# Performance work log

Measured on AMD Instinct MI355X. Metric: run time of the kernel, lower is better.

## Reference

```python
import jax, jax.numpy as jnp
import numpy as np

GAMMA = 0.999      # EMA momentum
M_PROTO = 10       # prototypes per class
K_CLS = 201        # 200 classes + background
EPS_SK = 0.05      # sinkhorn temperature
SK_ITERS = 3       # sinkhorn iterations
THR = 0.5          # pseudo-gt threshold
D_BB = 768         # backbone dim
D = 512            # projected dim


def _ln(x, g, b, eps=1e-5):
    mu = x.mean(-1, keepdims=True)
    var = ((x - mu) ** 2).mean(-1, keepdims=True)
    return (x - mu) / jnp.sqrt(var + eps) * g + b


def _l2n(x, eps=1e-12):
    n = jnp.linalg.norm(x, axis=-1, keepdims=True)
    return x / jnp.maximum(n, eps)


def _pca_dir(A, niter=10):
    # rank-1 PCA direction (deterministic power iteration; mirrors torch.pca_lowrank(q=1, center=True))
    Ac = A - A.mean(0, keepdims=True)
    v = jnp.ones((A.shape[1],), A.dtype) / jnp.sqrt(jnp.asarray(A.shape[1], A.dtype))
    for _ in range(niter):
        v = Ac.T @ (Ac @ v)
        v = v / jnp.linalg.norm(v)
    u = Ac @ v
    return u / jnp.linalg.norm(u)


def setup_inputs() -> dict:
    key = jax.random.key(0)
    ks = jax.random.split(key, 6)
    B, HW = 16, 1024
    return dict(
        patch_tokens=jax.random.normal(ks[0], (B, HW, D_BB), jnp.float32),
        gt=jax.random.randint(ks[1], (B,), 0, K_CLS - 1),
        proj_w=jax.random.normal(ks[2], (D, D_BB), jnp.float32) * 0.02,
        proj_b=jnp.zeros((D,), jnp.float32),
        feat_g=jnp.ones((D,), jnp.float32),
        feat_b=jnp.zeros((D,), jnp.float32),
        mask_g=jnp.ones((K_CLS,), jnp.float32),
        mask_b=jnp.zeros((K_CLS,), jnp.float32),
        prototypes=jax.random.normal(ks[3], (K_CLS, M_PROTO, D), jnp.float32) * 0.02,
    )


def reference(patch_tokens, gt, proj_w, proj_b, feat_g, feat_b, mask_g, mask_b, prototypes):
    B, HW, _ = patch_tokens.shape
    H = W = int(np.sqrt(HW))
    N = B * HW

    # ----- ged_pseudo_gt (on detached tokens) -----
    U = _pca_dir(patch_tokens.reshape(-1, D_BB))            # [N]
    Us = (U - U.min()) / (U.max() - U.min())
    Us = Us.reshape(B, H, W)
    pseudo_gt = jnp.where(Us < THR, gt[:, None, None], K_CLS - 1)  # [B,H,W]

    # ----- projection + normalization -----
    f = patch_tokens @ proj_w.T + proj_b                    # [B,HW,D]
    _c = _l2n(_ln(f.reshape(N, D), feat_g, feat_b))         # [N,D]
    protos = _l2n(prototypes)                               # buffer is l2-normalized in-place
    masks = jnp.einsum('nd,kmd->nmk', _c, protos)           # [N,M,K] cosine sims
    out_flat = _ln(masks.max(axis=1), mask_g, mask_b)       # [N,K]
    out_seg = out_flat.reshape(B, H, W, K_CLS).transpose(0, 3, 1, 2)  # [B,K,H,W]

    # ----- prototype_learning (vectorized 201-class loop) -----
    gt_seg = pseudo_gt.reshape(-1)                          # [N] int
    pred = jnp.argmax(out_flat, axis=-1)
    correct = (gt_seg == pred).astype(_c.dtype)             # [N]
    proto_logits = _c @ protos.reshape(-1, D).T             # [N, K*M]

    sel = jax.nn.one_hot(gt_seg, K_CLS, dtype=_c.dtype)     # [N,K] class membership
    Bk = sel.sum(0)                                         # pixels per class
    Bk_safe = jnp.where(Bk > 0, Bk, 1.0)

    # masked per-class sinkhorn (all classes in parallel)
    Q = jnp.exp(masks / EPS_SK) * sel[:, None, :]           # [N,M,K]
    sQ = Q.sum((0, 1))                                      # [K]
    Q = Q / jnp.where(sQ > 0, sQ, 1.0)
    for _ in range(SK_ITERS):
        row = Q.sum(0, keepdims=True)                       # [1,M,K] sum over pixels
        Q = Q / jnp.where(row > 0, row, 1.0) / M_PROTO
        col = Q.sum(1, keepdims=True)                       # [N,1,K] sum over prototypes
        Q = Q / jnp.where(col > 0, col, 1.0) / Bk_safe
    Q = Q * Bk                                              # [N,M,K]

    Qn = jnp.take_along_axis(Q, gt_seg[:, None, None], axis=2)[:, :, 0]  # [N,M]
    idx = jnp.argmax(Qn, axis=1)                            # hard assignment per pixel
    proto_target = (idx + M_PROTO * gt_seg).astype(jnp.float32)

    # EMA update: q masked by prediction correctness (m_k applies to both m_q and c_q; m_k^2 = m_k)
    q = jax.nn.one_hot(idx, M_PROTO, dtype=_c.dtype) * correct[:, None]  # [N,M]
    fproto = jnp.einsum('nk,nm,nd->kmd', sel, q, _c)        # per-(class,proto) feature sums
    ncnt = jnp.einsum('nk,nm->km', sel, q)                  # assignment counts
    fnorm = _l2n(fproto)
    upd = (ncnt != 0)[:, :, None]
    new_protos = _l2n(jnp.where(upd, GAMMA * protos + (1.0 - GAMMA) * fnorm, protos))

    return out_seg, proto_logits, proto_target, pseudo_gt, new_protos
```

## Files before the change

kernel.cpp:

```cpp
#include <hip/hip_runtime.h>
#include <cstdint>
#include <cstddef>

typedef _Float16 half8  __attribute__((ext_vector_type(8)));
typedef _Float16 half4v __attribute__((ext_vector_type(4)));
typedef float    f32x4  __attribute__((ext_vector_type(4)));

static constexpr int HWPX = 1024;
static constexpr int NPX  = 16384;
static constexpr int DBB  = 768;
static constexpr int DD   = 512;
static constexpr int KC   = 201;
static constexpr int KM   = 2010;
static constexpr int KMP  = 2048;

static constexpr size_t OFF_MEANP  = 0;
static constexpr size_t OFF_XCH    = 49152;
static constexpr size_t OFF_ROW16  = 540672;
static constexpr size_t OFF_ROW3   = 669696;
static constexpr size_t OFF_ROW5   = 677760;
static constexpr size_t OFF_BK     = 685824;
static constexpr size_t OFF_NCNT   = 686848;
static constexpr size_t OFF_FPROTO = 694912;
static constexpr size_t ZTOTAL     = 4811392;
static constexpr size_t OFF_MSF    = 4811392;
static constexpr size_t OFF_GTSEG  = 4817536;
static constexpr size_t OFF_CORR   = 4883072;
static constexpr size_t OFF_U      = 4948608;
static constexpr size_t OFF_PN     = 5079680;
static constexpr size_t OFF_P16    = 9196160;
static constexpr size_t OFF_C16    = 11293312;
static constexpr size_t OFF_QD     = 28070528;
static constexpr size_t OFF_W16    = 28725888;

static constexpr size_t OUT_SEG = 0;
static constexpr size_t OUT_PL  = 3293184;
static constexpr size_t OUT_PT  = 36225024;
static constexpr size_t OUT_PG  = 36241408;
static constexpr size_t OUT_NP  = 36257792;

#define GLDS16(gp, lp) __builtin_amdgcn_global_load_lds( \
    (__attribute__((address_space(1))) const void*)(gp), \
    (__attribute__((address_space(3))) void*)(lp), 16, 0, 0)

static __device__ __forceinline__ float  wredf(float x){
  #pragma unroll
  for (int o=32;o;o>>=1) x += __shfl_down(x,o);
  return x;
}
static __device__ __forceinline__ double wredd(double x){
  #pragma unroll
  for (int o=32;o;o>>=1) x += __shfl_down(x,o);
  return x;
}

__global__ __launch_bounds__(256) void kP0(const float* __restrict__ A, double* __restrict__ meanp){
  __shared__ double red[4][12][64];
  int lane = threadIdx.x & 63, w = threadIdx.x >> 6;
  int rbase = blockIdx.x*16 + w*4;
  double acc[12];
  #pragma unroll
  for (int j=0;j<12;j++) acc[j]=0.0;
  for (int i=0;i<4;i++){
    const float* Ar = A + (size_t)(rbase+i)*DBB;
    #pragma unroll
    for (int j=0;j<12;j++) acc[j] += (double)Ar[j*64+lane];
  }
  #pragma unroll
  for (int j=0;j<12;j++) red[w][j][lane] = acc[j];
  __syncthreads();
  double* dst = meanp + (size_t)(blockIdx.x&7)*768;
  for (int cc=threadIdx.x; cc<768; cc+=256){
    int j = cc>>6, l = cc&63;
    atomicAdd(&dst[cc], red[0][j][l]+red[1][j][l]+red[2][j][l]+red[3][j][l]);
  }
}

__global__ __launch_bounds__(256) void kRedM(const double* __restrict__ meanp, double* __restrict__ msf){
  for (int cc=threadIdx.x; cc<768; cc+=256){
    double s=0.0;
    #pragma unroll
    for (int p=0;p<8;p++) s += meanp[p*768+cc];
    msf[cc] = s * (1.0/16384.0);
  }
}

__global__ __launch_bounds__(256) void kPIter(const float* __restrict__ A, const double* __restrict__ msf,
                                              const double* __restrict__ xp, double* __restrict__ y){
  __shared__ double vs[768], ms[768];
  __shared__ double red[4][12][64];
  for (int cc=threadIdx.x; cc<768; cc+=256){
    ms[cc] = msf[cc];
    if (xp){
      double sv=0.0;
      #pragma unroll
      for (int p=0;p<8;p++) sv += xp[p*768+cc];
      vs[cc] = sv;
    } else {
      vs[cc] = 1.0/sqrt(768.0);
    }
  }
  __syncthreads();
  int lane = threadIdx.x & 63, w = threadIdx.x >> 6;
  int rbase = blockIdx.x*16 + w*4;
  double acc[12];
  #pragma unroll
  for (int j=0;j<12;j++) acc[j]=0.0;
  for (int i=0;i<4;i++){
    const float* Ar = A + (size_t)(rbase+i)*DBB;
    double ad[12]; double wp = 0.0;
    #pragma unroll
    for (int j=0;j<12;j++){ int c=j*64+lane; ad[j] = (double)Ar[c]-ms[c]; wp += ad[j]*vs[c]; }
    wp = wredd(wp); wp = __shfl(wp, 0);
    #pragma unroll
    for (int j=0;j<12;j++) acc[j] += wp*ad[j];
  }
  #pragma unroll
  for (int j=0;j<12;j++) red[w][j][lane] = acc[j];
  __syncthreads();
  double* dst = y + (size_t)(blockIdx.x&7)*768;
  for (int cc=threadIdx.x; cc<768; cc+=256){
    int j = cc>>6, l = cc&63;
    atomicAdd(&dst[cc], red[0][j][l]+red[1][j][l]+red[2][j][l]+red[3][j][l]);
  }
}

__global__ __launch_bounds__(256) void kPU(const float* __restrict__ A, const double* __restrict__ msf,
                                           const double* __restrict__ vp, double* __restrict__ u){
  __shared__ double vs[768], ms[768];
  for (int cc=threadIdx.x; cc<768; cc+=256){
    ms[cc] = msf[cc];
    double sv=0.0;
    #pragma unroll
    for (int p=0;p<8;p++) sv += vp[p*768+cc];
    vs[cc] = sv;
  }
  __syncthreads();
  int lane=threadIdx.x&63, w=threadIdx.x>>6;
  int rbase = blockIdx.x*16 + w*4;
  for (int i=0;i<4;i++){
    const float* Ar = A + (size_t)(rbase+i)*DBB;
    double wp=0.0;
    #pragma unroll
    for (int j=0;j<12;j++){ int c=j*64+lane; wp += ((double)Ar[c]-ms[c])*vs[c]; }
    wp = wredd(wp);
    if (lane==0) u[rbase+i] = wp;
  }
}

__global__ __launch_bounds__(1024) void kFin(const double* __restrict__ u, const int* __restrict__ gt,
      float* __restrict__ outPG, int* __restrict__ gtseg, int* __restrict__ Bk){
  __shared__ double smn[16], smx[16];
  __shared__ double sres[2];
  int t = threadIdx.x;
  double mn=1e300, mx=-1e300;
  for (int k=0;k<16;k++){ double x=u[k*1024+t]; mn=fmin(mn,x); mx=fmax(mx,x); }
  #pragma unroll
  for (int o=32;o;o>>=1){ mn=fmin(mn,__shfl_down(mn,o)); mx=fmax(mx,__shfl_down(mx,o)); }
  if ((t&63)==0){ smn[t>>6]=mn; smx[t>>6]=mx; }
  __syncthreads();
  if (t==0){
    for (int i=1;i<16;i++){ mn=fmin(mn,smn[i]); mx=fmax(mx,smx[i]); }
    sres[0]=mn; sres[1]=mx;
  }
  __syncthreads();
  mn=sres[0]; mx=sres[1];
  double inv = 1.0/(mx-mn);
  for (int k=0;k<16;k++){
    int n = k*1024 + t;
    int c0 = gt[k];
    double us = (u[n]-mn)*inv;
    int g = (us < 0.5) ? c0 : 200;
    outPG[n] = (float)g;
    gtseg[n] = g;
    unsigned long long b0 = __ballot(g==c0);
    unsigned long long b1 = __ballot(g==200);
    if ((t&63)==0){
      atomicAdd(&Bk[c0], (int)__popcll(b0));
      atomicAdd(&Bk[200], (int)__popcll(b1));
    }
  }
}

__global__ __launch_bounds__(256) void kPrep(const float* __restrict__ Wp, _Float16* __restrict__ W16,
    const float* __restrict__ PR, float* __restrict__ Pn, _Float16* __restrict__ P16){
  int b = blockIdx.x;
  if (b < 384){
    int i = b*256 + threadIdx.x;
    float4 vv = ((const float4*)Wp)[i];
    half4v h; h[0]=(_Float16)vv.x; h[1]=(_Float16)vv.y; h[2]=(_Float16)vv.z; h[3]=(_Float16)vv.w;
    ((half4v*)W16)[i] = h;
    return;
  }
  int w=threadIdx.x>>6, lane=threadIdx.x&63;
  int km = (b-384)*4 + w;
  if (km >= KM){
    if (km < KMP){
      half8 z;
      #pragma unroll
      for (int i=0;i<8;i++) z[i]=(_Float16)0.0f;
      *(half8*)(P16 + (size_t)km*DD + lane*8) = z;
    }
    return;
  }
  const float* r = PR + (size_t)km*DD + lane*8;
  float4 a = *(const float4*)r, b2 = *(const float4*)(r+4);
  float x[8] = {a.x,a.y,a.z,a.w,b2.x,b2.y,b2.z,b2.w};
  float ss=0;
  #pragma unroll
  for (int i=0;i<8;i++) ss += x[i]*x[i];
  ss = __shfl(wredf(ss),0);
  float nrm = fmaxf(sqrtf(ss), 1e-12f);
  float* pw = Pn + (size_t)km*DD + lane*8;
  half8 h;
  #pragma unroll
  for (int i=0;i<8;i++){ float vv = x[i]/nrm; pw[i]=vv; h[i]=(_Float16)vv; }
  *(half8*)(P16 + (size_t)km*DD + lane*8) = h;
}

__global__ __launch_bounds__(256) void gemm1(const float* __restrict__ Af, const _Float16* __restrict__ Bm,
    _Float16* __restrict__ Ch, const float* __restrict__ bias){
  __shared__ __align__(16) char As[128*128];
  __shared__ __align__(16) char Bs[128*128];
  const int tid = threadIdx.x;
  const int lane = tid & 63, w = tid >> 6;
  const int wr = w >> 1, wc = w & 1;
  const int lrow = lane & 15, kg = lane >> 4;
  const int id = blockIdx.x;
  const int xcd = id & 7, pos = id >> 3;
  const int m0 = ((xcd<<4) | (pos>>2)) * 128;
  const int n0 = (pos & 3) * 128;

  f32x4 acc[4][4];
  #pragma unroll
  for (int i=0;i<4;i++)
    #pragma unroll
    for (int j=0;j<4;j++){ f32x4 z = {0.f,0.f,0.f,0.f}; acc[i][j]=z; }

  for (int k0 = 0; k0 < DBB; k0 += 64){
    #pragma unroll
    for (int i=0;i<4;i++){
      int slot = (i*4 + w)*64 + lane;
      int r = slot >> 3, c = slot & 7;
      int cs = c ^ (r & 7);
      GLDS16(Bm + (size_t)(n0+r)*DBB + k0 + cs*8, Bs + (i*4+w)*1024);
    }
    #pragma unroll
    for (int i=0;i<8;i++){
      int slot = i*256 + tid;
      int r = slot >> 4, c4 = slot & 15;
      float4 v = *(const float4*)(Af + (size_t)(m0+r)*DBB + k0 + c4*4);
      half4v h; h[0]=(_Float16)v.x; h[1]=(_Float16)v.y; h[2]=(_Float16)v.z; h[3]=(_Float16)v.w;
      *(half4v*)(As + r*128 + (((c4>>1)^(r&7))<<4) + (c4&1)*8) = h;
    }
    __syncthreads();
    #pragma unroll
    for (int h=0; h<2; h++){
      half8 af[4], bf[4];
      #pragma unroll
      for (int mi=0;mi<4;mi++){
        int ar = wr*64 + mi*16 + lrow;
        af[mi] = *(const half8*)(As + ar*128 + (((h*4+kg) ^ (ar&7))<<4));
      }
      #pragma unroll
      for (int nj=0;nj<4;nj++){
        int br = wc*64 + nj*16 + lrow;
        bf[nj] = *(const half8*)(Bs + br*128 + (((h*4+kg) ^ (br&7))<<4));
      }
      #pragma unroll
      for (int mi=0;mi<4;mi++)
        #pragma unroll
        for (int nj=0;nj<4;nj++)
          acc[mi][nj] = __builtin_amdgcn_mfma_f32_16x16x32_f16(af[mi], bf[nj], acc[mi][nj], 0,0,0);
    }
    __syncthreads();
  }
  #pragma unroll
  for (int mi=0;mi<4;mi++){
    int gr = m0 + wr*64 + mi*16 + kg*4;
    #pragma unroll
    for (int nj=0;nj<4;nj++){
      int gc = n0 + wc*64 + nj*16 + lrow;
      float bv = bias[gc];
      #pragma unroll
      for (int r2=0;r2<4;r2++)
        Ch[(size_t)(gr+r2)*DD + gc] = (_Float16)(acc[mi][nj][r2] + bv);
    }
  }
}

__global__ __launch_bounds__(256) void gemm2(const _Float16* __restrict__ Am, const _Float16* __restrict__ Bm,
    float* __restrict__ Cf){
  __shared__ __align__(16) char As[128*128];
  __shared__ __align__(16) char Bs[128*128];
  const int tid = threadIdx.x;
  const int lane = tid & 63, w = tid >> 6;
  const int wr = w >> 1, wc = w & 1;
  const int lrow = lane & 15, kg = lane >> 4;
  const int id = blockIdx.x;
  const int xcd = id & 7, pos = id >> 3;
  const int m0 = ((xcd<<4) | (pos>>4)) * 128;
  const int n0 = (pos & 15) * 128;

  f32x4 acc[4][4];
  #pragma unroll
  for (int i=0;i<4;i++)
    #pragma unroll
    for (int j=0;j<4;j++){ f32x4 z = {0.f,0.f,0.f,0.f}; acc[i][j]=z; }

  for (int k0 = 0; k0 < DD; k0 += 64){
    #pragma unroll
    for (int i=0;i<4;i++){
      int slot = (i*4 + w)*64 + lane;
      int r = slot >> 3, c = slot & 7;
      int cs = c ^ (r & 7);
      GLDS16(Am + (size_t)(m0+r)*DD + k0 + cs*8, As + (i*4+w)*1024);
      GLDS16(Bm + (size_t)(n0+r)*DD + k0 + cs*8, Bs + (i*4+w)*1024);
    }
    __syncthreads();
    #pragma unroll
    for (int h=0; h<2; h++){
      half8 af[4], bf[4];
      #pragma unroll
      for (int mi=0;mi<4;mi++){
        int ar = wr*64 + mi*16 + lrow;
        af[mi] = *(const half8*)(As + ar*128 + (((h*4+kg) ^ (ar&7))<<4));
      }
      #pragma unroll
      for (int nj=0;nj<4;nj++){
        int br = wc*64 + nj*16 + lrow;
        bf[nj] = *(const half8*)(Bs + br*128 + (((h*4+kg) ^ (br&7))<<4));
      }
      #pragma unroll
      for (int mi=0;mi<4;mi++)
        #pragma unroll
        for (int nj=0;nj<4;nj++)
          acc[mi][nj] = __builtin_amdgcn_mfma_f32_16x16x32_f16(af[mi], bf[nj], acc[mi][nj], 0,0,0);
    }
    __syncthreads();
  }
  #pragma unroll
  for (int mi=0;mi<4;mi++){
    int gr = m0 + wr*64 + mi*16 + kg*4;
    #pragma unroll
    for (int nj=0;nj<4;nj++){
      int gc = n0 + wc*64 + nj*16 + lrow;
      if (gc < KM){
        #pragma unroll
        for (int r2=0;r2<4;r2++)
          Cf[(size_t)(gr+r2)*KM + gc] = acc[mi][nj][r2];
      }
    }
  }
}

__global__ __launch_bounds__(256) void kLNl2n(_Float16* __restrict__ C16,
      const float* __restrict__ fg, const float* __restrict__ fb){
  int w=threadIdx.x>>6, lane=threadIdx.x&63;
  int n = blockIdx.x*4 + w;
  _Float16* row = C16 + (size_t)n*DD + lane*8;
  half8 h = *(const half8*)row;
  float x[8];
  #pragma unroll
  for (int i=0;i<8;i++) x[i] = (float)h[i];
  float s=0;
  #pragma unroll
  for (int i=0;i<8;i++) s += x[i];
  float mu = __shfl(wredf(s),0)/512.f;
  float q=0;
  #pragma unroll
  for (int i=0;i<8;i++){ float d=x[i]-mu; q+=d*d; }
  float var = __shfl(wredf(q),0)/512.f;
  float inv = 1.f/sqrtf(var+1e-5f);
  float4 g0 = *(const float4*)(fg+lane*8), g1 = *(const float4*)(fg+lane*8+4);
  float4 b0 = *(const float4*)(fb+lane*8), b1 = *(const float4*)(fb+lane*8+4);
  float gg[8] = {g0.x,g0.y,g0.z,g0.w,g1.x,g1.y,g1.z,g1.w};
  float bb[8] = {b0.x,b0.y,b0.z,b0.w,b1.x,b1.y,b1.z,b1.w};
  float y[8]; float ss=0;
  #pragma unroll
  for (int i=0;i<8;i++){ y[i] = (x[i]-mu)*inv*gg[i]+bb[i]; ss += y[i]*y[i]; }
  float nrm = fmaxf(sqrtf(__shfl(wredf(ss),0)), 1e-12f);
  half8 o;
  #pragma unroll
  for (int i=0;i<8;i++) o[i] = (_Float16)(y[i]/nrm);
  *(half8*)row = o;
}

__global__ __launch_bounds__(256) void kMaxSK(const float* __restrict__ PL, const float* __restrict__ mg,
    const float* __restrict__ mb, const int* __restrict__ gtseg, const int* __restrict__ gt,
    float* __restrict__ outseg, int* __restrict__ corr, float* __restrict__ Qd, float* __restrict__ row16){
  __shared__ float rowb[4][2016];
  __shared__ float tile[32][205];
  int w=threadIdx.x>>6, lane=threadIdx.x&63;
  int n0 = blockIdx.x*32;
  int b = n0>>10, hw0 = n0&1023;
  int c0 = gt[b];
  float p0=0.f, p1=0.f;
  for (int g8=0; g8<8; ++g8){
    int n = n0 + g8*4 + w;
    int g = gtseg[n];
    const float* src = PL + (size_t)n*KM;
    for (int j2=lane;j2<1005;j2+=64)
      *(float2*)(&rowb[w][j2*2]) = *(const float2*)(src + j2*2);
    float xv[4]; int ncl=0;
    for (int c=lane;c<KC;c+=64){
      float mx = rowb[w][c*10];
      #pragma unroll
      for (int m=1;m<10;m++) mx = fmaxf(mx, rowb[w][c*10+m]);
      xv[ncl++] = mx;
    }
    float ps=0;
    for (int i=0;i<ncl;i++) ps += xv[i];
    float mu = __shfl(wredf(ps),0)*(1.f/201.f);
    float pv=0;
    for (int i=0;i<ncl;i++){ float d=xv[i]-mu; pv+=d*d; }
    float var = __shfl(wredf(pv),0)*(1.f/201.f);
    float inv = 1.f/sqrtf(var+1e-5f);
    float bv = -3.0e38f; int bi = 1<<30;
    int lr = g8*4 + w;
    ncl = 0;
    for (int c=lane;c<KC;c+=64){
      float o = (xv[ncl]-mu)*inv*mg[c]+mb[c]; ncl++;
      tile[lr][c] = o;
      if (o > bv){ bv=o; bi=c; }
    }
    #pragma unroll
    for (int o2=32;o2;o2>>=1){
      float ov = __shfl_down(bv,o2); int oi = __shfl_down(bi,o2);
      if (ov>bv || (ov==bv && oi<bi)){ bv=ov; bi=oi; }
    }
    if (lane==0) corr[n] = (bi==gtseg[n]) ? 1 : 0;
    if (lane < 10){
      float e = expf(rowb[w][g*10+lane]*20.f);
      Qd[(size_t)n*10+lane] = e;
      if (g==c0) p0 += e; else p1 += e;
    }
  }
  if (lane < 10){
    float* rp = row16 + (size_t)(blockIdx.x&15)*2016 + lane*KC;
    atomicAdd(&rp[c0], p0);
    atomicAdd(&rp[200], p1);
  }
  __syncthreads();
  for (int idx=threadIdx.x; idx<KC*32; idx+=256){
    int c = idx>>5, j = idx&31;
    outseg[(((size_t)b*KC+c)<<10) + hw0 + j] = tile[j][c];
  }
}

__global__ __launch_bounds__(256) void kSKpass(float* __restrict__ Qd, const int* __restrict__ gtseg,
      const int* __restrict__ gt, const float* __restrict__ rin, int rin_parts,
      float* __restrict__ rout, const int* __restrict__ Bk){
  __shared__ float rin2[10][2];
  __shared__ double part[4][10][2];
  int n = blockIdx.x*256+threadIdx.x;
  int c0 = gt[blockIdx.x>>2];
  if (threadIdx.x < 20){
    int m = threadIdx.x>>1, cl = threadIdx.x&1;
    int cls = cl?200:c0;
    float s=0;
    for (int p=0;p<rin_parts;p++) s += rin[(size_t)p*2016 + m*KC + cls];
    rin2[m][cl]=s;
  }
  __syncthreads();
  int g = gtseg[n];
  int cl = (g==200)?1:0;
  double q[10]; double col=0.0;
  #pragma unroll
  for (int m=0;m<10;m++){
    double r = (double)rin2[m][cl];
    double t = (double)Qd[(size_t)n*10+m];
    if (r>0.0) t = t/r;
    t = t/10.0;
    q[m]=t; col+=t;
  }
  double cs = (col>0.0)? col : 1.0;
  int bk = Bk[g];
  double bs = (bk>0)? (double)bk : 1.0;
  double inv = 1.0/(cs*bs);
  int w=threadIdx.x>>6, lane=threadIdx.x&63;
  #pragma unroll
  for (int m=0;m<10;m++){
    double t = q[m]*inv;
    Qd[(size_t)n*10+m] = (float)t;
    double p0 = (g==c0)? t:0.0;
    double p1 = (g==200)? t:0.0;
    p0=wredd(p0); p1=wredd(p1);
    if (lane==0){ part[w][m][0]=p0; part[w][m][1]=p1; }
  }
  __syncthreads();
  if (threadIdx.x < 20){
    int m = threadIdx.x>>1, cl2 = threadIdx.x&1;
    double t = part[0][m][cl2]+part[1][m][cl2]+part[2][m][cl2]+part[3][m][cl2];
    atomicAdd(&rout[m*KC + (cl2?200:c0)], (float)t);
  }
}

__global__ __launch_bounds__(256) void kSKEMA(const float* __restrict__ Qd, const int* __restrict__ gtseg,
      const float* __restrict__ r5, const int* __restrict__ corr, const _Float16* __restrict__ C16,
      float* __restrict__ outPT, float* __restrict__ fproto, int* __restrict__ ncnt){
  int w=threadIdx.x>>6, lane=threadIdx.x&63;
  int n = blockIdx.x*4+w;
  int g = gtseg[n];
  float tv = -1.0f;
  if (lane<10){
    float r = r5[lane*KC+g];
    float t = Qd[(size_t)n*10+lane];
    if (r>0.f) t = t/r;
    tv = t*0.1f;
  }
  float bv = tv; int bi = lane;
  #pragma unroll
  for (int o=8;o;o>>=1){
    float ov = __shfl_down(bv,o); int oi = __shfl_down(bi,o);
    if (ov>bv || (ov==bv && oi<bi)){ bv=ov; bi=oi; }
  }
  bi = __shfl(bi, 0);
  if (lane==0) outPT[n] = (float)(bi + 10*g);
  if (corr[n]){
    half8 hc = *(const half8*)(C16 + (size_t)n*DD + lane*8);
    float* dst = fproto + ((size_t)g*10+bi)*DD + lane*8;
    #pragma unroll
    for (int i=0;i<8;i++) atomicAdd(dst+i, (float)hc[i]);
    if (lane==0) atomicAdd(&ncnt[g*10+bi], 1);
  }
}

__global__ __launch_bounds__(256) void kEMAfin(const float* __restrict__ fproto, const int* __restrict__ ncnt,
     const float* __restrict__ Pn, float* __restrict__ outNP){
  int w=threadIdx.x>>6, lane=threadIdx.x&63;
  int km = blockIdx.x*4+w;
  if (km>=KM) return;
  const float* fr = fproto + (size_t)km*DD + lane*8;
  float fp[8]; float ss=0;
  #pragma unroll
  for (int i=0;i<8;i++){ fp[i]=fr[i]; ss+=fp[i]*fp[i]; }
  float n1 = fmaxf(sqrtf(__shfl(wredf(ss),0)), 1e-12f);
  int cnt = ncnt[km];
  const float* pr = Pn + (size_t)km*DD + lane*8;
  float t[8]; float s2=0;
  #pragma unroll
  for (int i=0;i<8;i++){
    float pv = pr[i];
    float tv = cnt ? (0.999f*pv + 0.001f*(fp[i]/n1)) : pv;
    t[i]=tv; s2+=tv*tv;
  }
  float n2 = fmaxf(sqrtf(__shfl(wredf(s2),0)), 1e-12f);
  float* dst = outNP + (size_t)km*DD + lane*8;
  #pragma unroll
  for (int i=0;i<8;i++) dst[i] = t[i]/n2;
}

extern "C" void kernel_launch(void* const* d_in, const int* in_sizes, int n_in,
                              void* d_out, int out_size, void* d_ws, size_t ws_size,
                              hipStream_t stream) {
  const float* A   = (const float*)d_in[0];
  const int*   gt  = (const int*)d_in[1];
  const float* Wp  = (const float*)d_in[2];
  const float* pb  = (const float*)d_in[3];
  const float* fg  = (const float*)d_in[4];
  const float* fb  = (const float*)d_in[5];
  const float* mg  = (const float*)d_in[6];
  const float* mb  = (const float*)d_in[7];
  const float* PR  = (const float*)d_in[8];
  float* out = (float*)d_out;
  char* ws = (char*)d_ws;

  double* meanp  = (double*)(ws+OFF_MEANP);
  double* xch    = (double*)(ws+OFF_XCH);
  float*  row16  = (float*)(ws+OFF_ROW16);
  float*  row3   = (float*)(ws+OFF_ROW3);
  float*  row5   = (float*)(ws+OFF_ROW5);
  int*    Bk     = (int*)(ws+OFF_BK);
  int*    ncnt   = (int*)(ws+OFF_NCNT);
  float*  fproto = (float*)(ws+OFF_FPROTO);
  double* msf    = (double*)(ws+OFF_MSF);
  int*    gtseg  = (int*)(ws+OFF_GTSEG);
  int*    corr   = (int*)(ws+OFF_CORR);
  double* u      = (double*)(ws+OFF_U);
  float*  Pn     = (float*)(ws+OFF_PN);
  _Float16* P16  = (_Float16*)(ws+OFF_P16);
  _Float16* C16  = (_Float16*)(ws+OFF_C16);
  float*  Qd     = (float*)(ws+OFF_QD);
  _Float16* W16  = (_Float16*)(ws+OFF_W16);

  hipMemsetAsync(ws, 0, ZTOTAL, stream);

  kP0<<<1024,256,0,stream>>>(A, meanp);
  kRedM<<<1,256,0,stream>>>(meanp, msf);
  for (int t=0;t<10;t++){
    const double* xp = (t==0)? nullptr : (xch + (size_t)(t-1)*8*768);
    kPIter<<<1024,256,0,stream>>>(A, msf, xp, xch + (size_t)t*8*768);
  }
  kPU<<<1024,256,0,stream>>>(A, msf, xch + (size_t)9*8*768, u);
  kFin<<<1,1024,0,stream>>>(u, gt, out+OUT_PG, gtseg, Bk);

  kPrep<<<896,256,0,stream>>>(Wp, W16, PR, Pn, P16);

  gemm1<<<512,256,0,stream>>>(A, W16, C16, pb);
  kLNl2n<<<4096,256,0,stream>>>(C16, fg, fb);

  gemm2<<<2048,256,0,stream>>>(C16, P16, out+OUT_PL);

  kMaxSK<<<512,256,0,stream>>>(out+OUT_PL, mg, mb, gtseg, gt, out+OUT_SEG, corr, Qd, row16);

  kSKpass<<<64,256,0,stream>>>(Qd, gtseg, gt, row16, 16, row3, Bk);
  kSKpass<<<64,256,0,stream>>>(Qd, gtseg, gt, row3, 1, row5, Bk);
  kSKEMA<<<4096,256,0,stream>>>(Qd, gtseg, row5, corr, C16, out+OUT_PT, fproto, ncnt);

  kEMAfin<<<503,256,0,stream>>>(fproto, ncnt, Pn, out+OUT_NP);
}
```

Measured before the change: 394.9 us.

## Fold mean-centering into power iteration and restructure max-pool kernel

```diff
diff --git a/kernel.cpp b/kernel.cpp
--- a/kernel.cpp
+++ b/kernel.cpp
@@ -14,24 +14,24 @@
 static constexpr int KM   = 2010;
 static constexpr int KMP  = 2048;
 
-static constexpr size_t OFF_MEANP  = 0;
-static constexpr size_t OFF_XCH    = 49152;
-static constexpr size_t OFF_ROW16  = 540672;
-static constexpr size_t OFF_ROW3   = 669696;
-static constexpr size_t OFF_ROW5   = 677760;
-static constexpr size_t OFF_BK     = 685824;
-static constexpr size_t OFF_NCNT   = 686848;
-static constexpr size_t OFF_FPROTO = 694912;
-static constexpr size_t ZTOTAL     = 4811392;
-static constexpr size_t OFF_MSF    = 4811392;
-static constexpr size_t OFF_GTSEG  = 4817536;
-static constexpr size_t OFF_CORR   = 4883072;
-static constexpr size_t OFF_U      = 4948608;
-static constexpr size_t OFF_PN     = 5079680;
-static constexpr size_t OFF_P16    = 9196160;
-static constexpr size_t OFF_C16    = 11293312;
-static constexpr size_t OFF_QD     = 28070528;
-static constexpr size_t OFF_W16    = 28725888;
+static constexpr size_t OFF_XCH    = 0;
+static constexpr size_t OFF_TP     = 491520;
+static constexpr size_t OFF_COLP   = 492160;
+static constexpr size_t OFF_ROW16  = 541312;
+static constexpr size_t OFF_ROW3   = 670336;
+static constexpr size_t OFF_ROW5   = 678400;
+static constexpr size_t OFF_BK     = 686464;
+static constexpr size_t OFF_NCNT   = 687488;
+static constexpr size_t OFF_FPROTO = 695552;
+static constexpr size_t ZTOTAL     = 4812032;
+static constexpr size_t OFF_GTSEG  = 4812032;
+static constexpr size_t OFF_CORR   = 4877568;
+static constexpr size_t OFF_U      = 4943104;
+static constexpr size_t OFF_PN     = 5074176;
+static constexpr size_t OFF_P16    = 9190656;
+static constexpr size_t OFF_C16    = 11287808;
+static constexpr size_t OFF_QD     = 28065024;
+static constexpr size_t OFF_W16    = 28720384;
 
 static constexpr size_t OUT_SEG = 0;
 static constexpr size_t OUT_PL  = 3293184;
@@ -54,97 +54,99 @@
   return x;
 }
 
-__global__ __launch_bounds__(256) void kP0(const float* __restrict__ A, double* __restrict__ meanp){
+template<bool FIRST>
+__global__ __launch_bounds__(256) void kPIter2(const float* __restrict__ A,
+    const double* __restrict__ Win, const double* __restrict__ Tin, const double* __restrict__ colp,
+    double* __restrict__ Wout, double* __restrict__ Tout, double* __restrict__ colout){
+  __shared__ double vs[768];
   __shared__ double red[4][12][64];
-  int lane = threadIdx.x & 63, w = threadIdx.x >> 6;
+  __shared__ double sT[4];
+  int tid=threadIdx.x, lane=tid&63, w=tid>>6;
+  if (FIRST){
+    for (int cc=tid; cc<768; cc+=256) vs[cc] = 1.0/sqrt(768.0);
+  } else {
+    double Ts=0.0;
+    #pragma unroll
+    for (int p=0;p<8;p++) Ts += Tin[p];
+    for (int cc=tid; cc<768; cc+=256){
+      double sw=0.0, mc=0.0;
+      #pragma unroll
+      for (int p=0;p<8;p++){ sw += Win[p*768+cc]; mc += colp[p*768+cc]; }
+      vs[cc] = sw - mc*(1.0/16384.0)*Ts;
+    }
+  }
+  __syncthreads();
   int rbase = blockIdx.x*16 + w*4;
-  double acc[12];
-  #pragma unroll
-  for (int j=0;j<12;j++) acc[j]=0.0;
+  double acc[12], cacc[12]; double tloc=0.0;
+  #pragma unroll
+  for (int j=0;j<12;j++){ acc[j]=0.0; cacc[j]=0.0; }
   for (int i=0;i<4;i++){
     const float* Ar = A + (size_t)(rbase+i)*DBB;
-    #pragma unroll
-    for (int j=0;j<12;j++) acc[j] += (double)Ar[j*64+lane];
-  }
-  #pragma unroll
-  for (int j=0;j<12;j++) red[w][j][lane] = acc[j];
-  __syncthreads();
-  double* dst = meanp + (size_t)(blockIdx.x&7)*768;
-  for (int cc=threadIdx.x; cc<768; cc+=256){
-    int j = cc>>6, l = cc&63;
+    double a[12]; double wp=0.0;
+    #pragma unroll
+    for (int j=0;j<12;j++){ int c=j*64+lane; a[j]=(double)Ar[c]; wp += a[j]*vs[c]; }
+    wp = wredd(wp); wp = __shfl(wp,0);
+    #pragma unroll
+    for (int j=0;j<12;j++) acc[j] += wp*a[j];
+    if (FIRST){
+      #pragma unroll
+      for (int j=0;j<12;j++) cacc[j] += a[j];
+    }
+    tloc += wp;
+  }
+  #pragma unroll
+  for (int j=0;j<12;j++) red[w][j][lane]=acc[j];
+  if (lane==0) sT[w]=tloc;
+  __syncthreads();
+  double* dst = Wout + (size_t)(blockIdx.x&7)*768;
+  for (int cc=tid; cc<768; cc+=256){
+    int j=cc>>6, l=cc&63;
     atomicAdd(&dst[cc], red[0][j][l]+red[1][j][l]+red[2][j][l]+red[3][j][l]);
   }
-}
-
-__global__ __launch_bounds__(256) void kRedM(const double* __restrict__ meanp, double* __restrict__ msf){
-  for (int cc=threadIdx.x; cc<768; cc+=256){
-    double s=0.0;
-    #pragma unroll
-    for (int p=0;p<8;p++) s += meanp[p*768+cc];
-    msf[cc] = s * (1.0/16384.0);
-  }
-}
-
-__global__ __launch_bounds__(256) void kPIter(const float* __restrict__ A, const double* __restrict__ msf,
-                                              const double* __restrict__ xp, double* __restrict__ y){
-  __shared__ double vs[768], ms[768];
-  __shared__ double red[4][12][64];
-  for (int cc=threadIdx.x; cc<768; cc+=256){
-    ms[cc] = msf[cc];
-    if (xp){
-      double sv=0.0;
-      #pragma unroll
-      for (int p=0;p<8;p++) sv += xp[p*768+cc];
-      vs[cc] = sv;
-    } else {
-      vs[cc] = 1.0/sqrt(768.0);
-    }
-  }
-  __syncthreads();
-  int lane = threadIdx.x & 63, w = threadIdx.x >> 6;
-  int rbase = blockIdx.x*16 + w*4;
-  double acc[12];
-  #pragma unroll
-  for (int j=0;j<12;j++) acc[j]=0.0;
-  for (int i=0;i<4;i++){
-    const float* Ar = A + (size_t)(rbase+i)*DBB;
-    double ad[12]; double wp = 0.0;
-    #pragma unroll
-    for (int j=0;j<12;j++){ int c=j*64+lane; ad[j] = (double)Ar[c]-ms[c]; wp += ad[j]*vs[c]; }
-    wp = wredd(wp); wp = __shfl(wp, 0);
-    #pragma unroll
-    for (int j=0;j<12;j++) acc[j] += wp*ad[j];
-  }
-  #pragma unroll
-  for (int j=0;j<12;j++) red[w][j][lane] = acc[j];
-  __syncthreads();
-  double* dst = y + (size_t)(blockIdx.x&7)*768;
-  for (int cc=threadIdx.x; cc<768; cc+=256){
-    int j = cc>>6, l = cc&63;
-    atomicAdd(&dst[cc], red[0][j][l]+red[1][j][l]+red[2][j][l]+red[3][j][l]);
-  }
-}
-
-__global__ __launch_bounds__(256) void kPU(const float* __restrict__ A, const double* __restrict__ msf,
-                                           const double* __restrict__ vp, double* __restrict__ u){
-  __shared__ double vs[768], ms[768];
-  for (int cc=threadIdx.x; cc<768; cc+=256){
-    ms[cc] = msf[cc];
-    double sv=0.0;
-    #pragma unroll
-    for (int p=0;p<8;p++) sv += vp[p*768+cc];
-    vs[cc] = sv;
-  }
-  __syncthreads();
-  int lane=threadIdx.x&63, w=threadIdx.x>>6;
+  if (tid==0) atomicAdd(&Tout[blockIdx.x&7], sT[0]+sT[1]+sT[2]+sT[3]);
+  if (FIRST){
+    __syncthreads();
+    #pragma unroll
+    for (int j=0;j<12;j++) red[w][j][lane]=cacc[j];
+    __syncthreads();
+    double* cdst = colout + (size_t)(blockIdx.x&7)*768;
+    for (int cc=tid; cc<768; cc+=256){
+      int j=cc>>6, l=cc&63;
+      atomicAdd(&cdst[cc], red[0][j][l]+red[1][j][l]+red[2][j][l]+red[3][j][l]);
+    }
+  }
+}
+
+__global__ __launch_bounds__(256) void kPU2(const float* __restrict__ A, const double* __restrict__ Wp,
+    const double* __restrict__ Tp, const double* __restrict__ colp, double* __restrict__ u){
+  __shared__ double vs[768];
+  __shared__ double sS[4];
+  int tid=threadIdx.x, lane=tid&63, w=tid>>6;
+  double Ts=0.0;
+  #pragma unroll
+  for (int p=0;p<8;p++) Ts += Tp[p];
+  double sloc=0.0;
+  for (int cc=tid; cc<768; cc+=256){
+    double sw=0.0, mc=0.0;
+    #pragma unroll
+    for (int p=0;p<8;p++){ sw += Wp[p*768+cc]; mc += colp[p*768+cc]; }
+    double m = mc*(1.0/16384.0);
+    double v = sw - m*Ts;
+    vs[cc] = v;
+    sloc += m*v;
+  }
+  sloc = wredd(sloc);
+  if (lane==0) sS[w]=sloc;
+  __syncthreads();
+  double s = sS[0]+sS[1]+sS[2]+sS[3];
   int rbase = blockIdx.x*16 + w*4;
   for (int i=0;i<4;i++){
     const float* Ar = A + (size_t)(rbase+i)*DBB;
     double wp=0.0;
     #pragma unroll
-    for (int j=0;j<12;j++){ int c=j*64+lane; wp += ((double)Ar[c]-ms[c])*vs[c]; }
+    for (int j=0;j<12;j++){ int c=j*64+lane; wp += (double)Ar[c]*vs[c]; }
     wp = wredd(wp);
-    if (lane==0) u[rbase+i] = wp;
+    if (lane==0) u[rbase+i] = wp - s;
   }
 }
 
@@ -389,26 +391,46 @@
 __global__ __launch_bounds__(256) void kMaxSK(const float* __restrict__ PL, const float* __restrict__ mg,
     const float* __restrict__ mb, const int* __restrict__ gtseg, const int* __restrict__ gt,
     float* __restrict__ outseg, int* __restrict__ corr, float* __restrict__ Qd, float* __restrict__ row16){
-  __shared__ float rowb[4][2016];
-  __shared__ float tile[32][205];
-  int w=threadIdx.x>>6, lane=threadIdx.x&63;
-  int n0 = blockIdx.x*32;
+  __shared__ float tile[16][205];
+  __shared__ float qpart[10][2];
+  int tid=threadIdx.x, lane=tid&63, w=tid>>6;
+  int n0 = blockIdx.x*16;
   int b = n0>>10, hw0 = n0&1023;
   int c0 = gt[b];
-  float p0=0.f, p1=0.f;
-  for (int g8=0; g8<8; ++g8){
-    int n = n0 + g8*4 + w;
+  if (tid<20) qpart[tid>>1][tid&1]=0.f;
+  __syncthreads();
+  for (int r=0;r<16;r++){
+    int n = n0 + r;
     int g = gtseg[n];
-    const float* src = PL + (size_t)n*KM;
-    for (int j2=lane;j2<1005;j2+=64)
-      *(float2*)(&rowb[w][j2*2]) = *(const float2*)(src + j2*2);
+    if (tid < KC){
+      const float* src = PL + (size_t)n*KM + tid*10;
+      float v[10];
+      #pragma unroll
+      for (int m2=0;m2<5;m2++){
+        float2 t2 = *(const float2*)(src + m2*2);
+        v[m2*2]=t2.x; v[m2*2+1]=t2.y;
+      }
+      float mx = v[0];
+      #pragma unroll
+      for (int m=1;m<10;m++) mx = fmaxf(mx,v[m]);
+      tile[r][tid] = mx;
+      if (tid == g){
+        int cl = (g==200)?1:0;
+        #pragma unroll
+        for (int m=0;m<10;m++){
+          float e = expf(v[m]*20.f);
+          Qd[(size_t)n*10+m] = e;
+          atomicAdd(&qpart[m][cl], e);
+        }
+      }
+    }
+  }
+  __syncthreads();
+  for (int rr=0; rr<4; ++rr){
+    int r = w*4 + rr;
+    int n = n0 + r;
     float xv[4]; int ncl=0;
-    for (int c=lane;c<KC;c+=64){
-      float mx = rowb[w][c*10];
-      #pragma unroll
-      for (int m=1;m<10;m++) mx = fmaxf(mx, rowb[w][c*10+m]);
-      xv[ncl++] = mx;
-    }
+    for (int c=lane;c<KC;c+=64) xv[ncl++] = tile[r][c];
     float ps=0;
     for (int i=0;i<ncl;i++) ps += xv[i];
     float mu = __shfl(wredf(ps),0)*(1.f/201.f);
@@ -416,34 +438,27 @@
     for (int i=0;i<ncl;i++){ float d=xv[i]-mu; pv+=d*d; }
     float var = __shfl(wredf(pv),0)*(1.f/201.f);
     float inv = 1.f/sqrtf(var+1e-5f);
-    float bv = -3.0e38f; int bi = 1<<30;
-    int lr = g8*4 + w;
-    ncl = 0;
+    float bv=-3.0e38f; int bi=1<<30;
+    ncl=0;
     for (int c=lane;c<KC;c+=64){
       float o = (xv[ncl]-mu)*inv*mg[c]+mb[c]; ncl++;
-      tile[lr][c] = o;
-      if (o > bv){ bv=o; bi=c; }
+      tile[r][c] = o;
+      if (o>bv){ bv=o; bi=c; }
     }
     #pragma unroll
     for (int o2=32;o2;o2>>=1){
-      float ov = __shfl_down(bv,o2); int oi = __shfl_down(bi,o2);
-      if (ov>bv || (ov==bv && oi<bi)){ bv=ov; bi=oi; }
-    }
-    if (lane==0) corr[n] = (bi==gtseg[n]) ? 1 : 0;
-    if (lane < 10){
-      float e = expf(rowb[w][g*10+lane]*20.f);
-      Qd[(size_t)n*10+lane] = e;
-      if (g==c0) p0 += e; else p1 += e;
-    }
-  }
-  if (lane < 10){
-    float* rp = row16 + (size_t)(blockIdx.x&15)*2016 + lane*KC;
-    atomicAdd(&rp[c0], p0);
-    atomicAdd(&rp[200], p1);
-  }
-  __syncthreads();
-  for (int idx=threadIdx.x; idx<KC*32; idx+=256){
-    int c = idx>>5, j = idx&31;
+      float ov=__shfl_down(bv,o2); int oi=__shfl_down(bi,o2);
+      if (ov>bv||(ov==bv&&oi<bi)){bv=ov;bi=oi;}
+    }
+    if (lane==0) corr[n] = (bi==gtseg[n])?1:0;
+  }
+  __syncthreads();
+  if (tid<20){
+    int m=tid>>1, cl=tid&1;
+    atomicAdd(&row16[(size_t)(blockIdx.x&15)*2016 + m*KC + (cl?200:c0)], qpart[m][cl]);
+  }
+  for (int idx=tid; idx<KC*16; idx+=256){
+    int c=idx>>4, j=idx&15;
     outseg[(((size_t)b*KC+c)<<10) + hw0 + j] = tile[j][c];
   }
 }
@@ -566,15 +581,15 @@
   float* out = (float*)d_out;
   char* ws = (char*)d_ws;
 
-  double* meanp  = (double*)(ws+OFF_MEANP);
   double* xch    = (double*)(ws+OFF_XCH);
+  double* Tp     = (double*)(ws+OFF_TP);
+  double* colp   = (double*)(ws+OFF_COLP);
   float*  row16  = (float*)(ws+OFF_ROW16);
   float*  row3   = (float*)(ws+OFF_ROW3);
   float*  row5   = (float*)(ws+OFF_ROW5);
   int*    Bk     = (int*)(ws+OFF_BK);
   int*    ncnt   = (int*)(ws+OFF_NCNT);
   float*  fproto = (float*)(ws+OFF_FPROTO);
-  double* msf    = (double*)(ws+OFF_MSF);
   int*    gtseg  = (int*)(ws+OFF_GTSEG);
   int*    corr   = (int*)(ws+OFF_CORR);
   double* u      = (double*)(ws+OFF_U);
@@ -586,13 +601,13 @@
 
   hipMemsetAsync(ws, 0, ZTOTAL, stream);
 
-  kP0<<<1024,256,0,stream>>>(A, meanp);
-  kRedM<<<1,256,0,stream>>>(meanp, msf);
-  for (int t=0;t<10;t++){
-    const double* xp = (t==0)? nullptr : (xch + (size_t)(t-1)*8*768);
-    kPIter<<<1024,256,0,stream>>>(A, msf, xp, xch + (size_t)t*8*768);
-  }
-  kPU<<<1024,256,0,stream>>>(A, msf, xch + (size_t)9*8*768, u);
+  kPIter2<true><<<1024,256,0,stream>>>(A, nullptr, nullptr, nullptr,
+                                       xch, Tp, colp);
+  for (int t=1;t<10;t++){
+    kPIter2<false><<<1024,256,0,stream>>>(A, xch+(size_t)(t-1)*8*768, Tp+(t-1)*8, colp,
+                                          xch+(size_t)t*8*768, Tp+t*8, nullptr);
+  }
+  kPU2<<<1024,256,0,stream>>>(A, xch+(size_t)9*8*768, Tp+9*8, colp, u);
   kFin<<<1,1024,0,stream>>>(u, gt, out+OUT_PG, gtseg, Bk);
 
   kPrep<<<896,256,0,stream>>>(Wp, W16, PR, Pn, P16);
@@ -602,7 +617,7 @@
 
   gemm2<<<2048,256,0,stream>>>(C16, P16, out+OUT_PL);
 
-  kMaxSK<<<512,256,0,stream>>>(out+OUT_PL, mg, mb, gtseg, gt, out+OUT_SEG, corr, Qd, row16);
+  kMaxSK<<<1024,256,0,stream>>>(out+OUT_PL, mg, mb, gtseg, gt, out+OUT_SEG, corr, Qd, row16);
 
   kSKpass<<<64,256,0,stream>>>(Qd, gtseg, gt, row16, 16, row3, Bk);
   kSKpass<<<64,256,0,stream>>>(Qd, gtseg, gt, row3, 1, row5, Bk);
```

Result: slower. 414.5 us (+5.0%).
